# Optimization experiments

Hardware: AMD Instinct MI355X
Metric: run time of the kernel (lower is better)

Reference implementation:

```python
import jax, jax.numpy as jnp
import numpy as np
import math

B, T, C, H = 4, 2048, 1024, 16
D = C // H  # head dim = 64
W_STD = 0.02


def setup_inputs() -> dict:
    key = jax.random.key(0)
    kx, kw, kb = jax.random.split(key, 3)
    x = jax.random.normal(kx, (B, T, C), dtype=jnp.float32)
    # Linear params stored as [in, 3*in] for x @ W; scaled like typical init
    w_qkv = jax.random.normal(kw, (C, 3 * C), dtype=jnp.float32) * W_STD
    b_qkv = jax.random.normal(kb, (3 * C,), dtype=jnp.float32) * W_STD
    return {"x": x, "w_qkv": w_qkv, "b_qkv": b_qkv}


def reference(x, w_qkv, b_qkv):
    # Fused QKV projection; torch splits as keys, queries, values (in that order)
    qkv = x @ w_qkv + b_qkv                      # [B, T, 3C]
    k, q, v = jnp.split(qkv, 3, axis=-1)          # each [B, T, C]

    def heads(t):  # [B, T, C] -> [B, H, T, D]
        return t.reshape(B, T, H, D).transpose(0, 2, 1, 3)

    k, q, v = heads(k), heads(q), heads(v)
    scale = 1.0 / math.sqrt(D)
    logits = jnp.einsum("bhqd,bhkd->bhqk", q, k) * scale  # [B, H, T, T]
    causal = jnp.tril(jnp.ones((T, T), dtype=bool))
    logits = jnp.where(causal, logits, -jnp.inf)
    probs = jax.nn.softmax(logits, axis=-1)
    y = jnp.einsum("bhqk,bhkd->bhqd", probs, v)   # [B, H, T, D]
    return y.transpose(0, 2, 1, 3).reshape(B, T, C)
```

## Files before the change

kernel.cpp:

```cpp
#include <hip/hip_runtime.h>
#include <hip/hip_bf16.h>

typedef unsigned short ushort_t;
typedef __attribute__((ext_vector_type(4))) short bf16x4_t;
typedef __attribute__((ext_vector_type(8))) short short8;
typedef __attribute__((ext_vector_type(4))) unsigned short ushort4_t;
typedef __attribute__((ext_vector_type(4))) float f32x4;
typedef __attribute__((ext_vector_type(2))) unsigned int uint2_t;
typedef __attribute__((ext_vector_type(4))) unsigned int uint4_t;

#define LOG2E 1.44269504088896340736f

__device__ __forceinline__ unsigned short f2bf(float f) {
    unsigned int u = __float_as_uint(f);
    u += 0x7fffu + ((u >> 16) & 1u);
    return (unsigned short)(u >> 16);
}

__device__ __forceinline__ unsigned int pk2bf(float a, float b) {
    union { __hip_bfloat162 h2; unsigned int u; } cvt;
    cvt.h2 = __float22bfloat162_rn(make_float2(a, b));
    return cvt.u;
}

__device__ __forceinline__ void gl_lds16(const ushort_t* g, ushort_t* l) {
    __builtin_amdgcn_global_load_lds(
        (const __attribute__((address_space(1))) unsigned int*)g,
        (__attribute__((address_space(3))) unsigned int*)l, 16, 0, 0);
}

__device__ __forceinline__ f32x4 mfma16(uint2_t a, uint2_t b, f32x4 c) {
    union { uint2_t u; bf16x4_t s; } ua, ub;
    ua.u = a; ub.u = b;
    return __builtin_amdgcn_mfma_f32_16x16x16bf16_1k(ua.s, ub.s, c, 0, 0, 0);
}

__global__ __launch_bounds__(256) void cvt_xw(
    const float* __restrict__ x, ushort_t* __restrict__ xb,
    const float* __restrict__ w, ushort_t* __restrict__ wt)
{
    __shared__ ushort_t Ts[64][40];
    const int bid = blockIdx.x;
    const int tid = threadIdx.x;
    if (bid < 4096) {
        const size_t i = ((size_t)bid * 256 + tid) * 8;
        const float4 a = *(const float4*)(x + i);
        const float4 b = *(const float4*)(x + i + 4);
        uint4_t o;
        o[0] = pk2bf(a.x, a.y); o[1] = pk2bf(a.z, a.w);
        o[2] = pk2bf(b.x, b.y); o[3] = pk2bf(b.z, b.w);
        *(uint4_t*)(xb + i) = o;
    } else {
        const int wb = bid - 4096;
        const int k0 = (wb & 31) * 32, n0 = (wb >> 5) * 64;
        const int kr = tid >> 3, nc = (tid & 7) * 8;
        const float* g = w + (size_t)(k0 + kr) * 3072 + n0 + nc;
        const float4 a = *(const float4*)g;
        const float4 b = *(const float4*)(g + 4);
        const float vals[8] = {a.x, a.y, a.z, a.w, b.x, b.y, b.z, b.w};
#pragma unroll
        for (int j = 0; j < 8; ++j) Ts[nc + j][kr] = f2bf(vals[j]);
        __syncthreads();
        const int nr = tid >> 2, kc = (tid & 3) * 8;
        const short8 v = *(const short8*)&Ts[nr][kc];
        *(short8*)(wt + (size_t)(n0 + nr) * 1024 + k0 + kc) = v;
    }
}

__global__ __launch_bounds__(256) void qkv_gemm(
    const ushort_t* __restrict__ xb, const ushort_t* __restrict__ wt,
    const float* __restrict__ bq,
    ushort_t* __restrict__ kws, ushort_t* __restrict__ qws,
    ushort_t* __restrict__ vws)
{
    __shared__ ushort_t As[3][128 * 32];
    __shared__ ushort_t Bs[3][128 * 32];

    const int tid  = threadIdx.x;
    const int m0   = blockIdx.x * 128;
    const int n0   = blockIdx.y * 128;
    const int wv   = tid >> 6;
    const int lane = tid & 63;
    const int qr   = lane & 15;
    const int quad = lane >> 4;
    const int wm   = (wv >> 1) * 64;
    const int wn   = (wv & 1) * 64;

    const int lr   = lane >> 2;
    const int csw  = (lane & 3) ^ ((lr >> 1) & 3);
    const ushort_t* gA = xb + (size_t)(m0 + wv*32 + lr) * 1024 + csw*8;
    const ushort_t* gB = wt + (size_t)(n0 + wv*32 + lr) * 1024 + csw*8;
    const int sdst = wv * 1024;

    const int swq = quad ^ ((qr >> 1) & 3);

    f32x4 acc[4][4];
#pragma unroll
    for (int i = 0; i < 4; ++i)
#pragma unroll
        for (int j = 0; j < 4; ++j) acc[i][j] = (f32x4){0.f, 0.f, 0.f, 0.f};

    gl_lds16(gA,             (ushort_t*)As + sdst);
    gl_lds16(gA + 16*1024,   (ushort_t*)As + sdst + 512);
    gl_lds16(gB,             (ushort_t*)Bs + sdst);
    gl_lds16(gB + 16*1024,   (ushort_t*)Bs + sdst + 512);
    gl_lds16(gA + 32,            (ushort_t*)As + 4096 + sdst);
    gl_lds16(gA + 32 + 16*1024,  (ushort_t*)As + 4096 + sdst + 512);
    gl_lds16(gB + 32,            (ushort_t*)Bs + 4096 + sdst);
    gl_lds16(gB + 32 + 16*1024,  (ushort_t*)Bs + 4096 + sdst + 512);

    int bufc = 0;
    for (int kt = 0; kt < 32; ++kt) {
        if (kt < 31) asm volatile("s_waitcnt vmcnt(4)" ::: "memory");
        else         asm volatile("s_waitcnt vmcnt(0)" ::: "memory");
        __builtin_amdgcn_s_barrier();
        __builtin_amdgcn_sched_barrier(0);

        const ushort_t* cA = (const ushort_t*)As + bufc * 4096;
        const ushort_t* cB = (const ushort_t*)Bs + bufc * 4096;
        short8 af[4], bfr[4];
#pragma unroll
        for (int i = 0; i < 4; ++i)
            af[i] = *(const short8*)&cA[(wm + i*16 + qr) * 32 + swq * 8];
#pragma unroll
        for (int j = 0; j < 4; ++j)
            bfr[j] = *(const short8*)&cB[(wn + j*16 + qr) * 32 + swq * 8];

        if (kt < 30) {
            int b2 = bufc + 2;
            if (b2 >= 3) b2 -= 3;
            const int k2 = (kt + 2) * 32;
            ushort_t* dA = (ushort_t*)As + b2 * 4096 + sdst;
            ushort_t* dB = (ushort_t*)Bs + b2 * 4096 + sdst;
            gl_lds16(gA + k2,            dA);
            gl_lds16(gA + k2 + 16*1024,  dA + 512);
            gl_lds16(gB + k2,            dB);
            gl_lds16(gB + k2 + 16*1024,  dB + 512);
        }

#pragma unroll
        for (int i = 0; i < 4; ++i)
#pragma unroll
            for (int j = 0; j < 4; ++j)
                acc[i][j] = __builtin_amdgcn_mfma_f32_16x16x32_bf16(
                    af[i], bfr[j], acc[i][j], 0, 0, 0);

        asm volatile("s_waitcnt lgkmcnt(0)" ::: "memory");
        bufc = (bufc == 2) ? 0 : bufc + 1;
    }

    const int nbase = n0 + wn;
    const int sec   = nbase >> 10;
    const int h     = (nbase & 1023) >> 6;

    if (sec == 2) {
#pragma unroll
        for (int j = 0; j < 4; ++j) {
            const float bias = bq[nbase + j*16 + qr];
            const int d = j*16 + qr;
#pragma unroll
            for (int i = 0; i < 4; ++i) {
                const int m  = m0 + wm + i*16 + quad*4;
                const int bb = m >> 11;
                const int tt = m & 2047;
                ushort4_t pk;
#pragma unroll
                for (int r = 0; r < 4; ++r) pk[r] = f2bf(acc[i][j][r] + bias);
                *(ushort4_t*)&vws[((size_t)(bb*16 + h)*64 + d)*2048 + tt] = pk;
            }
        }
    } else {
        ushort_t* __restrict__ dst = (sec == 0) ? kws : qws;
#pragma unroll
        for (int j = 0; j < 4; ++j) {
            const float bias = bq[nbase + j*16 + qr];
            const int d = j*16 + qr;
#pragma unroll
            for (int i = 0; i < 4; ++i) {
#pragma unroll
                for (int r = 0; r < 4; ++r) {
                    const int m  = m0 + wm + i*16 + quad*4 + r;
                    const int bb = m >> 11;
                    const int tt = m & 2047;
                    dst[(((size_t)(bb*16 + h)) * 2048 + tt) * 64 + d] =
                        f2bf(acc[i][j][r] + bias);
                }
            }
        }
    }
}

__global__ __launch_bounds__(256) void attn_fwd(
    const ushort_t* __restrict__ kws, const ushort_t* __restrict__ qws,
    const ushort_t* __restrict__ vws, float* __restrict__ out)
{
    constexpr int LDK = 72;
    __shared__ ushort_t Ks[2][64 * LDK];
    __shared__ ushort_t Vs[2][64 * LDK];

    const int tid  = threadIdx.x;
    const int wv   = tid >> 6;
    const int lane = tid & 63;
    const int qr   = lane & 15;
    const int quad = lane >> 4;
    const int srow = tid >> 2;
    const int scol = (tid & 3) * 16;
    constexpr float SCL = 0.125f * LOG2E;
    constexpr float CB  = 8.0f;

    const int bid = (int)blockIdx.x;
    const int qt  = 15 - (bid >> 6);
    const int bh  = bid & 63;
    const size_t bhT = (size_t)bh * 2048;
    const ushort_t* kbase = kws + bhT * 64;
    const ushort_t* vbase = vws + (size_t)bh * 64 * 2048;
    const int b = bh >> 4, h = bh & 15;

    const int q0   = qt * 128;
    const int base = q0 + wv*32;
    const int qv0  = base + qr;
    const int qv1  = qv0 + 16;

    const ushort_t* qg0 = qws + (bhT + qv0) * 64;
    const ushort_t* qg1 = qws + (bhT + qv1) * 64;
    const short8 Qb00 = *(const short8*)(qg0 + quad*8);
    const short8 Qb01 = *(const short8*)(qg0 + 32 + quad*8);
    const short8 Qb10 = *(const short8*)(qg1 + quad*8);
    const short8 Qb11 = *(const short8*)(qg1 + 32 + quad*8);

    float l_s[2] = {0.f, 0.f};
    f32x4 Oacc[2][4];
#pragma unroll
    for (int qs = 0; qs < 2; ++qs)
#pragma unroll
        for (int dt = 0; dt < 4; ++dt) Oacc[qs][dt] = (f32x4){0.f,0.f,0.f,0.f};

    const int nkt = 2*qt + 2;
    const int row_max = base + 31;

    short8 kv0, kv1, vv0, vv1;
    {
        const ushort_t* kg = kbase + (size_t)srow * 64 + scol;
        const ushort_t* vg = vbase + (size_t)srow * 2048 + scol;
        kv0 = *(const short8*)(kg);     kv1 = *(const short8*)(kg + 8);
        vv0 = *(const short8*)(vg);     vv1 = *(const short8*)(vg + 8);
    }
    *(short8*)&Ks[0][srow * LDK + scol]     = kv0;
    *(short8*)&Ks[0][srow * LDK + scol + 8] = kv1;
    *(short8*)&Vs[0][srow * LDK + scol]     = vv0;
    *(short8*)&Vs[0][srow * LDK + scol + 8] = vv1;
    __syncthreads();

    for (int kt = 0; kt < nkt; ++kt) {
        const int k0 = kt * 64;
        const int cur = kt & 1;
        const bool more = (kt + 1 < nkt);
        if (more) {
            const ushort_t* kg = kbase + (size_t)(k0 + 64 + srow) * 64 + scol;
            const ushort_t* vg = vbase + (size_t)srow * 2048 + k0 + 64 + scol;
            kv0 = *(const short8*)(kg);   kv1 = *(const short8*)(kg + 8);
            vv0 = *(const short8*)(vg);   vv1 = *(const short8*)(vg + 8);
        }

        if (k0 <= row_max) {
            const ushort_t* Kc = Ks[cur];
            const ushort_t* Vc = Vs[cur];
            const bool diag = (k0 + 63 > base);

            uint2_t pks[2][4];
            float ps0 = 0.f, ps1 = 0.f;
#pragma unroll
            for (int t4 = 0; t4 < 4; ++t4) {
                const short8 kf0 = *(const short8*)&Kc[(t4*16 + qr)*LDK + quad*8];
                const short8 kf1 = *(const short8*)&Kc[(t4*16 + qr)*LDK + 32 + quad*8];
                f32x4 a = (f32x4){0.f,0.f,0.f,0.f};
                f32x4 bfr = (f32x4){0.f,0.f,0.f,0.f};
                a   = __builtin_amdgcn_mfma_f32_16x16x32_bf16(kf0, Qb00, a, 0,0,0);
                a   = __builtin_amdgcn_mfma_f32_16x16x32_bf16(kf1, Qb01, a, 0,0,0);
                bfr = __builtin_amdgcn_mfma_f32_16x16x32_bf16(kf0, Qb10, bfr, 0,0,0);
                bfr = __builtin_amdgcn_mfma_f32_16x16x32_bf16(kf1, Qb11, bfr, 0,0,0);
                if (diag) {
#pragma unroll
                    for (int r = 0; r < 4; ++r) {
                        const int key = k0 + t4*16 + quad*4 + r;
                        if (key > qv0) a[r]   = -INFINITY;
                        if (key > qv1) bfr[r] = -INFINITY;
                    }
                }
                float p0[4], p1[4];
#pragma unroll
                for (int r = 0; r < 4; ++r) {
                    p0[r] = exp2f(__builtin_fmaf(a[r],   SCL, -CB));
                    p1[r] = exp2f(__builtin_fmaf(bfr[r], SCL, -CB));
                    ps0 += p0[r];
                    ps1 += p1[r];
                }
                pks[0][t4][0] = pk2bf(p0[0], p0[1]);
                pks[0][t4][1] = pk2bf(p0[2], p0[3]);
                pks[1][t4][0] = pk2bf(p1[0], p1[1]);
                pks[1][t4][1] = pk2bf(p1[2], p1[3]);
            }
            l_s[0] += ps0;
            l_s[1] += ps1;

            __builtin_amdgcn_s_setprio(1);
#pragma unroll
            for (int dt = 0; dt < 4; ++dt) {
#pragma unroll
                for (int t4 = 0; t4 < 4; ++t4) {
                    const uint2_t vf = *(const uint2_t*)
                        &Vc[(dt*16 + qr)*LDK + t4*16 + quad*4];
                    Oacc[0][dt] = mfma16(pks[0][t4], vf, Oacc[0][dt]);
                    Oacc[1][dt] = mfma16(pks[1][t4], vf, Oacc[1][dt]);
                }
            }
            __builtin_amdgcn_s_setprio(0);
        }

        if (more) {
            *(short8*)&Ks[cur ^ 1][srow * LDK + scol]     = kv0;
            *(short8*)&Ks[cur ^ 1][srow * LDK + scol + 8] = kv1;
            *(short8*)&Vs[cur ^ 1][srow * LDK + scol]     = vv0;
            *(short8*)&Vs[cur ^ 1][srow * LDK + scol + 8] = vv1;
        }
        __syncthreads();
    }

#pragma unroll
    for (int qs = 0; qs < 2; ++qs) {
        float lf = l_s[qs];
        lf += __shfl_xor(lf, 16);
        lf += __shfl_xor(lf, 32);
#pragma unroll
        for (int r = 0; r < 4; ++r) {
            const float lr  = __shfl(lf, quad*4 + r);
            const float inv = 1.f / lr;
            const int q = q0 + wv*32 + qs*16 + quad*4 + r;
            float* o = out + ((size_t)(b*2048 + q)) * 1024 + h*64;
#pragma unroll
            for (int dt = 0; dt < 4; ++dt) o[dt*16 + qr] = Oacc[qs][dt][r] * inv;
        }
    }
}

extern "C" void kernel_launch(void* const* d_in, const int* in_sizes, int n_in,
                              void* d_out, int out_size, void* d_ws, size_t ws_size,
                              hipStream_t stream) {
    (void)in_sizes; (void)n_in; (void)out_size; (void)ws_size;
    const float* x  = (const float*)d_in[0];
    const float* w  = (const float*)d_in[1];
    const float* bq = (const float*)d_in[2];
    float* out = (float*)d_out;

    ushort_t* kws = (ushort_t*)d_ws;
    ushort_t* qws = kws + (size_t)8388608;
    ushort_t* vws = qws + (size_t)8388608;
    ushort_t* xb  = vws + (size_t)8388608;
    ushort_t* wt  = xb  + (size_t)8388608;

    cvt_xw<<<5632, 256, 0, stream>>>(x, xb, w, wt);
    qkv_gemm<<<dim3(64, 24), 256, 0, stream>>>(xb, wt, bq, kws, qws, vws);
    attn_fwd<<<1024, 256, 0, stream>>>(kws, qws, vws, out);
}
```

Before: 225.4 us.

## Process key tiles in pairs per iteration and set occupancy launch bound

Restructures the attention loop to load and compute two 64-key tiles per iteration, prefetching the next pair into registers, so that barriers are amortized over more compute. Both LDS buffers are now consumed each iteration, and refilling them requires an extra barrier before the stores since double buffering across iterations is lost. Adds __launch_bounds__(256,4) to constrain registers for higher occupancy. This risks register spills and gives less overlap between the global loads and the LDS writes.

After: 249.3 us. 10.6% more time.

```diff
diff --git a/kernel.cpp b/kernel.cpp
--- a/kernel.cpp
+++ b/kernel.cpp
@@ -190,7 +190,7 @@
     }
 }
 
-__global__ __launch_bounds__(256) void attn_fwd(
+__global__ __launch_bounds__(256, 4) void attn_fwd(
     const ushort_t* __restrict__ kws, const ushort_t* __restrict__ qws,
     const ushort_t* __restrict__ vws, float* __restrict__ out)
 {
@@ -235,93 +235,109 @@
 #pragma unroll
         for (int dt = 0; dt < 4; ++dt) Oacc[qs][dt] = (f32x4){0.f,0.f,0.f,0.f};
 
-    const int nkt = 2*qt + 2;
+    const int npair  = qt + 1;
     const int row_max = base + 31;
 
-    short8 kv0, kv1, vv0, vv1;
+    auto computeTile = [&](const ushort_t* Kc, const ushort_t* Vc,
+                           const int k0) {
+        const bool diag = (k0 + 63 > base);
+        uint2_t pks[2][4];
+        float ps0 = 0.f, ps1 = 0.f;
+#pragma unroll
+        for (int t4 = 0; t4 < 4; ++t4) {
+            const short8 kf0 = *(const short8*)&Kc[(t4*16 + qr)*LDK + quad*8];
+            const short8 kf1 = *(const short8*)&Kc[(t4*16 + qr)*LDK + 32 + quad*8];
+            f32x4 a = (f32x4){0.f,0.f,0.f,0.f};
+            f32x4 bfr = (f32x4){0.f,0.f,0.f,0.f};
+            a   = __builtin_amdgcn_mfma_f32_16x16x32_bf16(kf0, Qb00, a, 0,0,0);
+            a   = __builtin_amdgcn_mfma_f32_16x16x32_bf16(kf1, Qb01, a, 0,0,0);
+            bfr = __builtin_amdgcn_mfma_f32_16x16x32_bf16(kf0, Qb10, bfr, 0,0,0);
+            bfr = __builtin_amdgcn_mfma_f32_16x16x32_bf16(kf1, Qb11, bfr, 0,0,0);
+            if (diag) {
+#pragma unroll
+                for (int r = 0; r < 4; ++r) {
+                    const int key = k0 + t4*16 + quad*4 + r;
+                    if (key > qv0) a[r]   = -INFINITY;
+                    if (key > qv1) bfr[r] = -INFINITY;
+                }
+            }
+            float p0[4], p1[4];
+#pragma unroll
+            for (int r = 0; r < 4; ++r) {
+                p0[r] = exp2f(__builtin_fmaf(a[r],   SCL, -CB));
+                p1[r] = exp2f(__builtin_fmaf(bfr[r], SCL, -CB));
+                ps0 += p0[r];
+                ps1 += p1[r];
+            }
+            pks[0][t4][0] = pk2bf(p0[0], p0[1]);
+            pks[0][t4][1] = pk2bf(p0[2], p0[3]);
+            pks[1][t4][0] = pk2bf(p1[0], p1[1]);
+            pks[1][t4][1] = pk2bf(p1[2], p1[3]);
+        }
+        l_s[0] += ps0;
+        l_s[1] += ps1;
+
+        __builtin_amdgcn_s_setprio(1);
+#pragma unroll
+        for (int dt = 0; dt < 4; ++dt) {
+#pragma unroll
+            for (int t4 = 0; t4 < 4; ++t4) {
+                const uint2_t vf = *(const uint2_t*)
+                    &Vc[(dt*16 + qr)*LDK + t4*16 + quad*4];
+                Oacc[0][dt] = mfma16(pks[0][t4], vf, Oacc[0][dt]);
+                Oacc[1][dt] = mfma16(pks[1][t4], vf, Oacc[1][dt]);
+            }
+        }
+        __builtin_amdgcn_s_setprio(0);
+    };
+
+    short8 ka0, ka1, va0, va1, kb0, kb1, vb0, vb1;
     {
-        const ushort_t* kg = kbase + (size_t)srow * 64 + scol;
-        const ushort_t* vg = vbase + (size_t)srow * 2048 + scol;
-        kv0 = *(const short8*)(kg);     kv1 = *(const short8*)(kg + 8);
-        vv0 = *(const short8*)(vg);     vv1 = *(const short8*)(vg + 8);
-    }
-    *(short8*)&Ks[0][srow * LDK + scol]     = kv0;
-    *(short8*)&Ks[0][srow * LDK + scol + 8] = kv1;
-    *(short8*)&Vs[0][srow * LDK + scol]     = vv0;
-    *(short8*)&Vs[0][srow * LDK + scol + 8] = vv1;
+        const ushort_t* kg0 = kbase + (size_t)srow * 64 + scol;
+        const ushort_t* vg0 = vbase + (size_t)srow * 2048 + scol;
+        ka0 = *(const short8*)(kg0);        ka1 = *(const short8*)(kg0 + 8);
+        va0 = *(const short8*)(vg0);        va1 = *(const short8*)(vg0 + 8);
+        kb0 = *(const short8*)(kg0 + 64*64);
+        kb1 = *(const short8*)(kg0 + 64*64 + 8);
+        vb0 = *(const short8*)(vg0 + 64);   vb1 = *(const short8*)(vg0 + 64 + 8);
+    }
+    *(short8*)&Ks[0][srow * LDK + scol]     = ka0;
+    *(short8*)&Ks[0][srow * LDK + scol + 8] = ka1;
+    *(short8*)&Vs[0][srow * LDK + scol]     = va0;
+    *(short8*)&Vs[0][srow * LDK + scol + 8] = va1;
+    *(short8*)&Ks[1][srow * LDK + scol]     = kb0;
+    *(short8*)&Ks[1][srow * LDK + scol + 8] = kb1;
+    *(short8*)&Vs[1][srow * LDK + scol]     = vb0;
+    *(short8*)&Vs[1][srow * LDK + scol + 8] = vb1;
     __syncthreads();
 
-    for (int kt = 0; kt < nkt; ++kt) {
-        const int k0 = kt * 64;
-        const int cur = kt & 1;
-        const bool more = (kt + 1 < nkt);
+    for (int p = 0; p < npair; ++p) {
+        const int k0 = p * 128;
+        const bool more = (p + 1 < npair);
         if (more) {
-            const ushort_t* kg = kbase + (size_t)(k0 + 64 + srow) * 64 + scol;
-            const ushort_t* vg = vbase + (size_t)srow * 2048 + k0 + 64 + scol;
-            kv0 = *(const short8*)(kg);   kv1 = *(const short8*)(kg + 8);
-            vv0 = *(const short8*)(vg);   vv1 = *(const short8*)(vg + 8);
-        }
-
-        if (k0 <= row_max) {
-            const ushort_t* Kc = Ks[cur];
-            const ushort_t* Vc = Vs[cur];
-            const bool diag = (k0 + 63 > base);
-
-            uint2_t pks[2][4];
-            float ps0 = 0.f, ps1 = 0.f;
-#pragma unroll
-            for (int t4 = 0; t4 < 4; ++t4) {
-                const short8 kf0 = *(const short8*)&Kc[(t4*16 + qr)*LDK + quad*8];
-                const short8 kf1 = *(const short8*)&Kc[(t4*16 + qr)*LDK + 32 + quad*8];
-                f32x4 a = (f32x4){0.f,0.f,0.f,0.f};
-                f32x4 bfr = (f32x4){0.f,0.f,0.f,0.f};
-                a   = __builtin_amdgcn_mfma_f32_16x16x32_bf16(kf0, Qb00, a, 0,0,0);
-                a   = __builtin_amdgcn_mfma_f32_16x16x32_bf16(kf1, Qb01, a, 0,0,0);
-                bfr = __builtin_amdgcn_mfma_f32_16x16x32_bf16(kf0, Qb10, bfr, 0,0,0);
-                bfr = __builtin_amdgcn_mfma_f32_16x16x32_bf16(kf1, Qb11, bfr, 0,0,0);
-                if (diag) {
-#pragma unroll
-                    for (int r = 0; r < 4; ++r) {
-                        const int key = k0 + t4*16 + quad*4 + r;
-                        if (key > qv0) a[r]   = -INFINITY;
-                        if (key > qv1) bfr[r] = -INFINITY;
-                    }
-                }
-                float p0[4], p1[4];
-#pragma unroll
-                for (int r = 0; r < 4; ++r) {
-                    p0[r] = exp2f(__builtin_fmaf(a[r],   SCL, -CB));
-                    p1[r] = exp2f(__builtin_fmaf(bfr[r], SCL, -CB));
-                    ps0 += p0[r];
-                    ps1 += p1[r];
-                }
-                pks[0][t4][0] = pk2bf(p0[0], p0[1]);
-                pks[0][t4][1] = pk2bf(p0[2], p0[3]);
-                pks[1][t4][0] = pk2bf(p1[0], p1[1]);
-                pks[1][t4][1] = pk2bf(p1[2], p1[3]);
-            }
-            l_s[0] += ps0;
-            l_s[1] += ps1;
-
-            __builtin_amdgcn_s_setprio(1);
-#pragma unroll
-            for (int dt = 0; dt < 4; ++dt) {
-#pragma unroll
-                for (int t4 = 0; t4 < 4; ++t4) {
-                    const uint2_t vf = *(const uint2_t*)
-                        &Vc[(dt*16 + qr)*LDK + t4*16 + quad*4];
-                    Oacc[0][dt] = mfma16(pks[0][t4], vf, Oacc[0][dt]);
-                    Oacc[1][dt] = mfma16(pks[1][t4], vf, Oacc[1][dt]);
-                }
-            }
-            __builtin_amdgcn_s_setprio(0);
-        }
-
+            const ushort_t* kg = kbase + (size_t)(k0 + 128 + srow) * 64 + scol;
+            const ushort_t* vg = vbase + (size_t)srow * 2048 + k0 + 128 + scol;
+            ka0 = *(const short8*)(kg);         ka1 = *(const short8*)(kg + 8);
+            va0 = *(const short8*)(vg);         va1 = *(const short8*)(vg + 8);
+            kb0 = *(const short8*)(kg + 64*64);
+            kb1 = *(const short8*)(kg + 64*64 + 8);
+            vb0 = *(const short8*)(vg + 64);    vb1 = *(const short8*)(vg + 64 + 8);
+        }
+
+        computeTile(Ks[0], Vs[0], k0);
+        if (k0 + 64 <= row_max)
+            computeTile(Ks[1], Vs[1], k0 + 64);
+
+        __syncthreads();
         if (more) {
-            *(short8*)&Ks[cur ^ 1][srow * LDK + scol]     = kv0;
-            *(short8*)&Ks[cur ^ 1][srow * LDK + scol + 8] = kv1;
-            *(short8*)&Vs[cur ^ 1][srow * LDK + scol]     = vv0;
-            *(short8*)&Vs[cur ^ 1][srow * LDK + scol + 8] = vv1;
+            *(short8*)&Ks[0][srow * LDK + scol]     = ka0;
+            *(short8*)&Ks[0][srow * LDK + scol + 8] = ka1;
+            *(short8*)&Vs[0][srow * LDK + scol]     = va0;
+            *(short8*)&Vs[0][srow * LDK + scol + 8] = va1;
+            *(short8*)&Ks[1][srow * LDK + scol]     = kb0;
+            *(short8*)&Ks[1][srow * LDK + scol + 8] = kb1;
+            *(short8*)&Vs[1][srow * LDK + scol]     = vb0;
+            *(short8*)&Vs[1][srow * LDK + scol + 8] = vb1;
         }
         __syncthreads();
     }
```
